# Kernel optimization log

Measured on AMD Instinct MI355X. Metric: run time of the kernel, lower is better.

## Reference

```python
import jax, jax.numpy as jnp
import numpy as np

B, OBS, T, H = 4096, 16, 32, 512  # batch, encoder length, decode seq_len, hidden_size


def _lstm_cell(x, h, c, Wi, Wh, b):
    # PyTorch gate order: i, f, g, o. b = b_ih + b_hh (mathematically identical).
    g = x @ Wi.T + h @ Wh.T + b
    i, f, gg, o = jnp.split(g, 4, axis=-1)
    c = jax.nn.sigmoid(f) * c + jax.nn.sigmoid(i) * jnp.tanh(gg)
    h = jax.nn.sigmoid(o) * jnp.tanh(c)
    return h, c


def _encode(xs, Wi, Wh, b):
    # xs: [B, T, 4]; returns final (h, c), zero initial state as in nn.LSTM.
    def step(carry, x):
        h, c = _lstm_cell(x, carry[0], carry[1], Wi, Wh, b)
        return (h, c), None
    z = jnp.zeros((xs.shape[0], H), xs.dtype)
    (h, c), _ = jax.lax.scan(step, (z, z), jnp.swapaxes(xs, 0, 1))
    return h, c


def setup_inputs() -> dict:
    key = jax.random.key(0)
    ks = jax.random.split(key, 22)
    s = 0.05
    p = lambda k, shape: (jax.random.normal(k, shape, jnp.float32) * s)
    return {
        "speed": jax.random.normal(ks[0], (B, OBS, 4), jnp.float32),
        "pos": jax.random.normal(ks[1], (B, OBS, 4), jnp.float32),
        "enc_s_Wi": p(ks[2], (4 * H, 4)), "enc_s_Wh": p(ks[3], (4 * H, H)), "enc_s_b": p(ks[4], (4 * H,)),
        "enc_p_Wi": p(ks[5], (4 * H, 4)), "enc_p_Wh": p(ks[6], (4 * H, H)), "enc_p_b": p(ks[7], (4 * H,)),
        "dec_s_Wi": p(ks[8], (4 * H, 4)), "dec_s_Wh": p(ks[9], (4 * H, H)), "dec_s_b": p(ks[10], (4 * H,)),
        "dec_i_Wi": p(ks[11], (4 * H, 4)), "dec_i_Wh": p(ks[12], (4 * H, H)), "dec_i_b": p(ks[13], (4 * H,)),
        "W_fs": p(ks[14], (4, H)), "b_fs": p(ks[15], (4,)),
        "W_fc": p(ks[16], (2, H)), "b_fc": p(ks[17], (2,)),
        "W_emb": p(ks[18], (4, 2)), "b_emb": p(ks[19], (4,)),
    }


def reference(speed, pos,
              enc_s_Wi, enc_s_Wh, enc_s_b,
              enc_p_Wi, enc_p_Wh, enc_p_b,
              dec_s_Wi, dec_s_Wh, dec_s_b,
              dec_i_Wi, dec_i_Wh, dec_i_b,
              W_fs, b_fs, W_fc, b_fc, W_emb, b_emb):
    h_se, c_se = _encode(speed, enc_s_Wi, enc_s_Wh, enc_s_b)
    h_pe, c_pe = _encode(pos, enc_p_Wi, enc_p_Wh, enc_p_b)
    h_s, c_s = h_se + h_pe, c_se + c_pe
    h_i, c_i = h_s, c_s
    last_speed = speed[:, -1, :]
    last_pos = pos[:, -1, :]

    def step(carry, _):
        h_s, c_s, h_i, c_i, ls, lp = carry
        h_s, c_s = _lstm_cell(ls, h_s, c_s, dec_s_Wi, dec_s_Wh, dec_s_b)
        h_i, c_i = _lstm_cell(lp, h_i, c_i, dec_i_Wi, dec_i_Wh, dec_i_b)
        sp = jnp.clip(h_s @ W_fs.T + b_fs, -100.0, 100.0)        # Hardtanh(-100, 100)
        it = jax.nn.relu(h_i @ W_fc.T + b_fc)                     # fc_crossing
        ls = jax.lax.stop_gradient(sp)                            # .detach()
        lp = jax.lax.stop_gradient(jax.nn.relu(it @ W_emb.T + b_emb))  # pos_embedding(.).detach()
        return (h_s, c_s, h_i, c_i, ls, lp), (sp, jax.nn.softmax(it, axis=1))

    carry0 = (h_s, c_s, h_i, c_i, last_speed, last_pos)
    _, (speed_seq, cross_seq) = jax.lax.scan(step, carry0, None, length=T)
    speed_outputs = jnp.swapaxes(speed_seq, 0, 1)   # [B, T, 4]
    # Faithful to the source bug: intention_outputs is never accumulated, so the
    # returned crossing_outputs holds ONLY the last step's softmax: [B, 1, 2].
    crossing_outputs = cross_seq[-1][:, None, :]
    return speed_outputs, crossing_outputs
```

## Files before the change

### kernel.cpp

```cpp
#include <hip/hip_runtime.h>
#include <stdint.h>

#define H 512
#define KAUG 528
#define KT_N 33
#define LROW 536
#define NROW 32
#define WMAT_ELEMS (16 * KT_N * 4 * 512)
#define WMAT8_BYTES 1081344
#define NTL8_BYTES 67584
#define T_DEC 32
#define B_TOT 4096
#define SCL 0.015625f

typedef __attribute__((ext_vector_type(8))) short short8;
typedef __attribute__((ext_vector_type(16))) float floatx16;
typedef __attribute__((ext_vector_type(2))) float float2v;
typedef __attribute__((ext_vector_type(4))) unsigned int uint4v;
typedef __attribute__((ext_vector_type(2))) unsigned int uint2v;

__device__ __forceinline__ unsigned short f2bf(float x) {
  union { float f; unsigned int u; } v; v.f = x;
  unsigned int u = v.u;
  return (unsigned short)((u + 0x7FFFu + ((u >> 16) & 1u)) >> 16);
}
__device__ __forceinline__ float bf2f(unsigned short s) {
  union { unsigned int u; float f; } v; v.u = ((unsigned int)s) << 16;
  return v.f;
}
__device__ __forceinline__ float rcpf(float x) { return __builtin_amdgcn_rcpf(x); }
__device__ __forceinline__ float sigm(float x) { return rcpf(1.0f + __expf(-x)); }
__device__ __forceinline__ float tanh_f(float x) {
  return 1.0f - 2.0f * rcpf(1.0f + __expf(2.0f * x));
}

__device__ __forceinline__ unsigned char f2e4m3(float f) {
  unsigned int u = __float_as_uint(f);
  unsigned int s = (u >> 24) & 0x80u;
  float a = fabsf(f);
  if (!(a < 464.0f)) return (unsigned char)(s | 0x7Eu);
  if (a < 0.0009765625f) return (unsigned char)s;
  int e = (int)((__float_as_uint(a) >> 23) & 0xFF) - 127;
  int q = (e < -6 ? -6 : e) - 3;
  float sc  = __uint_as_float((unsigned int)((127 - q) << 23));
  float isc = __uint_as_float((unsigned int)((127 + q) << 23));
  float n = rintf(a * sc);
  float r = n * isc;
  if (r == 0.0f) return (unsigned char)s;
  int e2 = (int)((__float_as_uint(r) >> 23) & 0xFF) - 127;
  unsigned int bits;
  if (e2 < -6) {
    bits = (unsigned int)(r * 512.0f + 0.5f);
  } else {
    float msc = __uint_as_float((unsigned int)((127 - (e2 - 3)) << 23));
    unsigned int mant = (unsigned int)(r * msc + 0.5f);
    bits = ((unsigned int)(e2 + 7) << 3) | (mant & 7u);
  }
  return (unsigned char)(s | bits);
}

__device__ __forceinline__ short8 dq8(unsigned int d0, unsigned int d1) {
  float2v p0 = __builtin_amdgcn_cvt_pk_f32_fp8(d0, false);
  float2v p1 = __builtin_amdgcn_cvt_pk_f32_fp8(d0, true);
  float2v p2 = __builtin_amdgcn_cvt_pk_f32_fp8(d1, false);
  float2v p3 = __builtin_amdgcn_cvt_pk_f32_fp8(d1, true);
  union { unsigned int u[4]; short8 s; } r;
  r.u[0] = __builtin_amdgcn_perm(__float_as_uint(p0[1]), __float_as_uint(p0[0]), 0x07060302u);
  r.u[1] = __builtin_amdgcn_perm(__float_as_uint(p1[1]), __float_as_uint(p1[0]), 0x07060302u);
  r.u[2] = __builtin_amdgcn_perm(__float_as_uint(p2[1]), __float_as_uint(p2[0]), 0x07060302u);
  r.u[3] = __builtin_amdgcn_perm(__float_as_uint(p3[1]), __float_as_uint(p3[0]), 0x07060302u);
  return r.s;
}

__global__ void prep_weights(
    const float* __restrict__ Wh_s, const float* __restrict__ Wi_s, const float* __restrict__ b_s,
    const float* __restrict__ Wh_p, const float* __restrict__ Wi_p, const float* __restrict__ b_p,
    short* __restrict__ wpack)
{
  int idx = blockIdx.x * 256 + threadIdx.x;
  const int per = 2048 * KAUG;
  if (idx >= 2 * per) return;
  int mat = idx / per;
  int rem = idx - mat * per;
  int n = rem / KAUG;
  int ka = rem - n * KAUG;
  const float* Wh = mat ? Wh_p : Wh_s;
  const float* Wi = mat ? Wi_p : Wi_s;
  const float* bb = mat ? b_p  : b_s;
  float v;
  if (ka < 512)      v = Wh[n * 512 + ka];
  else if (ka < 516) v = Wi[n * 4 + (ka - 512)];
  else if (ka == 516) v = bb[n];
  else               v = 0.0f;
  int g = n >> 9, ntL = (n >> 5) & 15, ni = n & 31;
  int kt = ka >> 4, kh = (ka >> 3) & 1, ks = ka & 7;
  int lanep = kh * 32 + ni;
  wpack[(size_t)mat * WMAT_ELEMS +
        (((((size_t)ntL * KT_N + kt) * 4 + g) << 9) + (lanep << 3) + ks)] = (short)f2bf(v);
}

__global__ void prep_fp8(
    const float* __restrict__ Wh_d, const float* __restrict__ Wi_d, const float* __restrict__ b_d,
    const float* __restrict__ Wh_i, const float* __restrict__ Wi_i, const float* __restrict__ b_i,
    unsigned char* __restrict__ wpack8)
{
  int idx = blockIdx.x * 256 + threadIdx.x;
  if (idx >= 2 * WMAT8_BYTES) return;
  int mat = idx / WMAT8_BYTES;
  int rem = idx - mat * WMAT8_BYTES;
  int ntL = rem / NTL8_BYTES;
  int off = rem - ntL * NTL8_BYTES;
  int g, lane, kt, ks;
  if (off < 65536) {
    int p = off >> 12;
    g = (off >> 10) & 3;
    lane = (off >> 4) & 63;
    int j = off & 15;
    kt = 2 * p + (j >> 3);
    ks = j & 7;
  } else {
    int t = off - 65536;
    g = t >> 9;
    lane = (t >> 3) & 63;
    ks = t & 7;
    kt = 32;
  }
  int n = g * 512 + ntL * 32 + (lane & 31);
  int ka = kt * 16 + (lane >> 5) * 8 + ks;
  const float* Wh = mat ? Wh_i : Wh_d;
  const float* Wi = mat ? Wi_i : Wi_d;
  const float* bb = mat ? b_i  : b_d;
  float v;
  if (ka < 512)       v = Wh[n * 512 + ka];
  else if (ka < 516)  v = Wi[n * 4 + (ka - 512)];
  else if (ka == 516) v = bb[n];
  else                v = 0.0f;
  wpack8[idx] = f2e4m3(v * 64.0f);
}

__device__ __forceinline__ void lstm_step_mfma(
    const short* hl, const short* __restrict__ wm,
    int lane, int wv, float c_reg[16], float hnew[16])
{
  int arow = lane & 31, ahalf = lane >> 5;
  const short* aptr = hl + arow * LROW + ahalf * 8;
  const short* bp = wm + (size_t)wv * (KT_N * 4 * 512) + (lane << 3);
  floatx16 ai = (floatx16)0.0f, af = (floatx16)0.0f, ag = (floatx16)0.0f, ao = (floatx16)0.0f;
  #pragma unroll 3
  for (int kt = 0; kt < KT_N; ++kt) {
    short8 a  = *(const short8*)(aptr + kt * 16);
    short8 b0 = *(const short8*)(bp);
    short8 b1 = *(const short8*)(bp + 512);
    short8 b2 = *(const short8*)(bp + 1024);
    short8 b3 = *(const short8*)(bp + 1536);
    bp += 2048;
    ai = __builtin_amdgcn_mfma_f32_32x32x16_bf16(a, b0, ai, 0, 0, 0);
    af = __builtin_amdgcn_mfma_f32_32x32x16_bf16(a, b1, af, 0, 0, 0);
    ag = __builtin_amdgcn_mfma_f32_32x32x16_bf16(a, b2, ag, 0, 0, 0);
    ao = __builtin_amdgcn_mfma_f32_32x32x16_bf16(a, b3, ao, 0, 0, 0);
  }
  #pragma unroll
  for (int r = 0; r < 16; ++r) {
    float si = sigm(ai[r]);
    float sf = sigm(af[r]);
    float tg = tanh_f(ag[r]);
    float so = sigm(ao[r]);
    float cn = sf * c_reg[r] + si * tg;
    c_reg[r] = cn;
    hnew[r] = so * tanh_f(cn);
  }
}

__device__ __forceinline__ void lstm_step_mfma_fp8(
    const short* hl, const unsigned char* __restrict__ wmb,
    int lane, int wv, float c_reg[16], float hnew[16])
{
  int arow = lane & 31, ahalf = lane >> 5;
  const short* aptr = hl + arow * LROW + ahalf * 8;
  const unsigned char* base = wmb + (size_t)wv * NTL8_BYTES;
  const uint4v* bp = (const uint4v*)(base + (lane << 4));
  floatx16 ai = (floatx16)0.0f, af = (floatx16)0.0f, ag = (floatx16)0.0f, ao = (floatx16)0.0f;
  #pragma unroll 1
  for (int p = 0; p < 16; ++p) {
    uint4v di = bp[0];
    uint4v df = bp[64];
    uint4v dg = bp[128];
    uint4v dd = bp[192];
    short8 a0 = *(const short8*)(aptr + p * 32);
    short8 a1 = *(const short8*)(aptr + p * 32 + 16);
    bp += 256;
    ai = __builtin_amdgcn_mfma_f32_32x32x16_bf16(a0, dq8(di[0], di[1]), ai, 0, 0, 0);
    af = __builtin_amdgcn_mfma_f32_32x32x16_bf16(a0, dq8(df[0], df[1]), af, 0, 0, 0);
    ag = __builtin_amdgcn_mfma_f32_32x32x16_bf16(a0, dq8(dg[0], dg[1]), ag, 0, 0, 0);
    ao = __builtin_amdgcn_mfma_f32_32x32x16_bf16(a0, dq8(dd[0], dd[1]), ao, 0, 0, 0);
    ai = __builtin_amdgcn_mfma_f32_32x32x16_bf16(a1, dq8(di[2], di[3]), ai, 0, 0, 0);
    af = __builtin_amdgcn_mfma_f32_32x32x16_bf16(a1, dq8(df[2], df[3]), af, 0, 0, 0);
    ag = __builtin_amdgcn_mfma_f32_32x32x16_bf16(a1, dq8(dg[2], dg[3]), ag, 0, 0, 0);
    ao = __builtin_amdgcn_mfma_f32_32x32x16_bf16(a1, dq8(dd[2], dd[3]), ao, 0, 0, 0);
  }
  {
    const uint2v* tp = (const uint2v*)(base + 65536 + (lane << 3));
    uint2v ti = tp[0], tf = tp[64], tg = tp[128], td = tp[192];
    short8 a0 = *(const short8*)(aptr + 512);
    ai = __builtin_amdgcn_mfma_f32_32x32x16_bf16(a0, dq8(ti[0], ti[1]), ai, 0, 0, 0);
    af = __builtin_amdgcn_mfma_f32_32x32x16_bf16(a0, dq8(tf[0], tf[1]), af, 0, 0, 0);
    ag = __builtin_amdgcn_mfma_f32_32x32x16_bf16(a0, dq8(tg[0], tg[1]), ag, 0, 0, 0);
    ao = __builtin_amdgcn_mfma_f32_32x32x16_bf16(a0, dq8(td[0], td[1]), ao, 0, 0, 0);
  }
  #pragma unroll
  for (int r = 0; r < 16; ++r) {
    float si = sigm(ai[r] * SCL);
    float sf = sigm(af[r] * SCL);
    float tg = tanh_f(ag[r] * SCL);
    float so = sigm(ao[r] * SCL);
    float cn = sf * c_reg[r] + si * tg;
    c_reg[r] = cn;
    hnew[r] = so * tanh_f(cn);
  }
}

__device__ __forceinline__ void write_h(short* hl, int lane, int wv, const float hnew[16]) {
  int arow = lane & 31, ahalf = lane >> 5;
  int col = (wv << 5) + arow;
  #pragma unroll
  for (int r = 0; r < 16; ++r) {
    int row = (r & 3) + ((r >> 2) << 3) + (ahalf << 2);
    hl[row * LROW + col] = (short)f2bf(hnew[r]);
  }
}

__global__ __launch_bounds__(1024) void lstm_encoder(
    const float* __restrict__ speed, const float* __restrict__ pos,
    const short* __restrict__ wpack,
    short* __restrict__ h_enc, float* __restrict__ c_enc)
{
  __shared__ short hl[NROW * LROW];
  int tid = threadIdx.x;
  int b = blockIdx.x;
  int xcd = b & 7, slot = b >> 3;
  int enc = xcd >> 2;
  int rg = slot * 4 + (xcd & 3);
  int r0 = rg * 32;
  const float* xin = enc ? pos : speed;
  const short* wm = wpack + (size_t)enc * WMAT_ELEMS;

  for (int i = tid; i < NROW * LROW; i += 1024) hl[i] = 0;
  __syncthreads();
  if (tid < 32) hl[tid * LROW + 516] = (short)0x3F80;
  if (tid < 128) {
    int r = tid >> 2, c = tid & 3;
    hl[r * LROW + 512 + c] = (short)f2bf(xin[(r0 + r) * 64 + c]);
  }
  __syncthreads();

  int lane = tid & 63, wv = tid >> 6;
  float c_reg[16];
  #pragma unroll
  for (int r = 0; r < 16; ++r) c_reg[r] = 0.0f;
  float hnew[16];

  for (int t = 0; t < 16; ++t) {
    lstm_step_mfma(hl, wm, lane, wv, c_reg, hnew);
    __syncthreads();
    write_h(hl, lane, wv, hnew);
    if (t < 15 && tid < 128) {
      int r = tid >> 2, c = tid & 3;
      hl[r * LROW + 512 + c] = (short)f2bf(xin[(r0 + r) * 64 + (t + 1) * 4 + c]);
    }
    __syncthreads();
  }

  for (int i = tid; i < 32 * 512; i += 1024) {
    int r = i >> 9, k = i & 511;
    h_enc[((size_t)(enc * B_TOT + r0 + r) << 9) + k] = hl[r * LROW + k];
  }
  int arow = lane & 31, ahalf = lane >> 5;
  int col = (wv << 5) + arow;
  #pragma unroll
  for (int r = 0; r < 16; ++r) {
    int row = (r & 3) + ((r >> 2) << 3) + (ahalf << 2);
    c_enc[((size_t)(enc * B_TOT + r0 + row) << 9) + col] = c_reg[r];
  }
}

__global__ __launch_bounds__(1024) void lstm_decoder(
    const float* __restrict__ speed, const float* __restrict__ pos,
    const unsigned char* __restrict__ wpack8,
    const short* __restrict__ h_enc, const float* __restrict__ c_enc,
    const float* __restrict__ W_fs, const float* __restrict__ b_fs,
    const float* __restrict__ W_fc, const float* __restrict__ b_fc,
    const float* __restrict__ W_emb, const float* __restrict__ b_emb,
    float* __restrict__ out)
{
  __shared__ short hl[NROW * LROW];
  int tid = threadIdx.x;
  int b = blockIdx.x;
  int xcd = b & 7, slot = b >> 3;
  int chain = xcd >> 2;
  int rg = slot * 4 + (xcd & 3);
  int r0 = rg * 32;
  const unsigned char* wm8 = wpack8 + (size_t)chain * WMAT8_BYTES;

  for (int i = tid; i < NROW * LROW; i += 1024) hl[i] = 0;
  __syncthreads();
  for (int i = tid; i < 32 * 512; i += 1024) {
    int r = i >> 9, k = i & 511;
    float h0 = bf2f((unsigned short)h_enc[((size_t)(r0 + r) << 9) + k])
             + bf2f((unsigned short)h_enc[((size_t)(B_TOT + r0 + r) << 9) + k]);
    hl[r * LROW + k] = (short)f2bf(h0);
  }
  if (tid < 32) hl[tid * LROW + 516] = (short)0x3F80;
  {
    const float* last = chain ? pos : speed;
    if (tid < 128) {
      int r = tid >> 2, c = tid & 3;
      hl[r * LROW + 512 + c] = (short)f2bf(last[(r0 + r) * 64 + 60 + c]);
    }
  }
  int lane = tid & 63, wv = tid >> 6;
  int arow = lane & 31, ahalf = lane >> 5;
  float c_reg[16];
  {
    int col = (wv << 5) + arow;
    #pragma unroll
    for (int r = 0; r < 16; ++r) {
      int row = (r & 3) + ((r >> 2) << 3) + (ahalf << 2);
      size_t gi = ((size_t)(r0 + row) << 9) + col;
      c_reg[r] = c_enc[gi] + c_enc[gi + (((size_t)B_TOT) << 9)];
    }
  }
  __syncthreads();

  float hnew[16];
  for (int t = 0; t < T_DEC; ++t) {
    lstm_step_mfma_fp8(hl, wm8, lane, wv, c_reg, hnew);
    __syncthreads();
    write_h(hl, lane, wv, hnew);
    __syncthreads();
    for (int r = 0; r < 2; ++r) {
      int row = wv * 2 + r;
      const short8 hvs = *(const short8*)(hl + row * LROW + lane * 8);
      float hv[8];
      #pragma unroll
      for (int j = 0; j < 8; ++j) hv[j] = bf2f((unsigned short)hvs[j]);
      if (chain == 0) {
        float p0 = 0.f, p1 = 0.f, p2 = 0.f, p3 = 0.f;
        #pragma unroll
        for (int j = 0; j < 8; ++j) {
          p0 += hv[j] * W_fs[0 * 512 + lane * 8 + j];
          p1 += hv[j] * W_fs[1 * 512 + lane * 8 + j];
          p2 += hv[j] * W_fs[2 * 512 + lane * 8 + j];
          p3 += hv[j] * W_fs[3 * 512 + lane * 8 + j];
        }
        #pragma unroll
        for (int off = 32; off > 0; off >>= 1) {
          p0 += __shfl_xor(p0, off);
          p1 += __shfl_xor(p1, off);
          p2 += __shfl_xor(p2, off);
          p3 += __shfl_xor(p3, off);
        }
        float s0 = fminf(fmaxf(p0 + b_fs[0], -100.0f), 100.0f);
        float s1 = fminf(fmaxf(p1 + b_fs[1], -100.0f), 100.0f);
        float s2 = fminf(fmaxf(p2 + b_fs[2], -100.0f), 100.0f);
        float s3 = fminf(fmaxf(p3 + b_fs[3], -100.0f), 100.0f);
        if (lane < 4) {
          float v = (lane == 0) ? s0 : (lane == 1) ? s1 : (lane == 2) ? s2 : s3;
          out[(size_t)(r0 + row) * 128 + t * 4 + lane] = v;
          hl[row * LROW + 512 + lane] = (short)f2bf(v);
        }
      } else {
        float p0 = 0.f, p1 = 0.f;
        #pragma unroll
        for (int j = 0; j < 8; ++j) {
          p0 += hv[j] * W_fc[0 * 512 + lane * 8 + j];
          p1 += hv[j] * W_fc[1 * 512 + lane * 8 + j];
        }
        #pragma unroll
        for (int off = 32; off > 0; off >>= 1) {
          p0 += __shfl_xor(p0, off);
          p1 += __shfl_xor(p1, off);
        }
        float it0 = fmaxf(p0 + b_fc[0], 0.0f);
        float it1 = fmaxf(p1 + b_fc[1], 0.0f);
        if (lane < 4) {
          float lp = fmaxf(W_emb[lane * 2] * it0 + W_emb[lane * 2 + 1] * it1 + b_emb[lane], 0.0f);
          hl[row * LROW + 512 + lane] = (short)f2bf(lp);
        }
        if (t == T_DEC - 1 && lane < 2) {
          float m = fmaxf(it0, it1);
          float e0 = __expf(it0 - m), e1 = __expf(it1 - m);
          float v = ((lane == 0) ? e0 : e1) * rcpf(e0 + e1);
          out[(size_t)524288 + (size_t)(r0 + row) * 2 + lane] = v;
        }
      }
    }
    __syncthreads();
  }
}

extern "C" void kernel_launch(void* const* d_in, const int* in_sizes, int n_in,
                              void* d_out, int out_size, void* d_ws, size_t ws_size,
                              hipStream_t stream)
{
  const float* speed    = (const float*)d_in[0];
  const float* pos      = (const float*)d_in[1];
  const float* enc_s_Wi = (const float*)d_in[2];
  const float* enc_s_Wh = (const float*)d_in[3];
  const float* enc_s_b  = (const float*)d_in[4];
  const float* enc_p_Wi = (const float*)d_in[5];
  const float* enc_p_Wh = (const float*)d_in[6];
  const float* enc_p_b  = (const float*)d_in[7];
  const float* dec_s_Wi = (const float*)d_in[8];
  const float* dec_s_Wh = (const float*)d_in[9];
  const float* dec_s_b  = (const float*)d_in[10];
  const float* dec_i_Wi = (const float*)d_in[11];
  const float* dec_i_Wh = (const float*)d_in[12];
  const float* dec_i_b  = (const float*)d_in[13];
  const float* W_fs     = (const float*)d_in[14];
  const float* b_fs     = (const float*)d_in[15];
  const float* W_fc     = (const float*)d_in[16];
  const float* b_fc     = (const float*)d_in[17];
  const float* W_emb    = (const float*)d_in[18];
  const float* b_emb    = (const float*)d_in[19];
  float* out = (float*)d_out;

  char* ws = (char*)d_ws;
  short* wpack          = (short*)ws;
  unsigned char* wpack8 = (unsigned char*)(ws + 4325376);
  short* h_enc          = (short*)(ws + 6488064);
  float* c_enc          = (float*)(ws + 14876672);

  prep_weights<<<8448, 256, 0, stream>>>(
      enc_s_Wh, enc_s_Wi, enc_s_b,
      enc_p_Wh, enc_p_Wi, enc_p_b,
      wpack);
  prep_fp8<<<8448, 256, 0, stream>>>(
      dec_s_Wh, dec_s_Wi, dec_s_b,
      dec_i_Wh, dec_i_Wi, dec_i_b,
      wpack8);
  lstm_encoder<<<256, 1024, 0, stream>>>(speed, pos, wpack, h_enc, c_enc);
  lstm_decoder<<<256, 1024, 0, stream>>>(speed, pos, wpack8, h_enc, c_enc,
                                         W_fs, b_fs, W_fc, b_fc, W_emb, b_emb, out);
}
```

Before: 1.377 ms.

## Split decoder into 16-row blocks with double-buffered hidden state

The decoder now launches 512 blocks of 512 threads instead of 256 of 1024. Each block handles 16 batch rows, and each wave computes two gate tiles. The hidden state is double-buffered in shared memory, so new h values are written straight into the next buffer and one barrier per step goes away. The trade-off is that the 32x32 MFMA tiles now carry only 16 valid rows (the rest are zero padding), and each block still streams the full FP8 weight matrix, so weight traffic and matrix work per useful row roughly double.

```diff
diff --git a/kernel.cpp b/kernel.cpp
--- a/kernel.cpp
+++ b/kernel.cpp
@@ -33,6 +33,8 @@
 __device__ __forceinline__ float tanh_f(float x) {
   return 1.0f - 2.0f * rcpf(1.0f + __expf(2.0f * x));
 }
+
+#define MFMA(A, B, C) __builtin_amdgcn_mfma_f32_32x32x16_bf16(A, B, C, 0, 0, 0)
 
 __device__ __forceinline__ unsigned char f2e4m3(float f) {
   unsigned int u = __float_as_uint(f);
@@ -72,7 +74,7 @@
   return r.s;
 }
 
-__global__ void prep_weights(
+__global__ void prep_enc(
     const float* __restrict__ Wh_s, const float* __restrict__ Wi_s, const float* __restrict__ b_s,
     const float* __restrict__ Wh_p, const float* __restrict__ Wi_p, const float* __restrict__ b_p,
     short* __restrict__ wpack)
@@ -154,10 +156,8 @@
     short8 b2 = *(const short8*)(bp + 1024);
     short8 b3 = *(const short8*)(bp + 1536);
     bp += 2048;
-    ai = __builtin_amdgcn_mfma_f32_32x32x16_bf16(a, b0, ai, 0, 0, 0);
-    af = __builtin_amdgcn_mfma_f32_32x32x16_bf16(a, b1, af, 0, 0, 0);
-    ag = __builtin_amdgcn_mfma_f32_32x32x16_bf16(a, b2, ag, 0, 0, 0);
-    ao = __builtin_amdgcn_mfma_f32_32x32x16_bf16(a, b3, ao, 0, 0, 0);
+    ai = MFMA(a, b0, ai); af = MFMA(a, b1, af);
+    ag = MFMA(a, b2, ag); ao = MFMA(a, b3, ao);
   }
   #pragma unroll
   for (int r = 0; r < 16; ++r) {
@@ -171,55 +171,7 @@
   }
 }
 
-__device__ __forceinline__ void lstm_step_mfma_fp8(
-    const short* hl, const unsigned char* __restrict__ wmb,
-    int lane, int wv, float c_reg[16], float hnew[16])
-{
-  int arow = lane & 31, ahalf = lane >> 5;
-  const short* aptr = hl + arow * LROW + ahalf * 8;
-  const unsigned char* base = wmb + (size_t)wv * NTL8_BYTES;
-  const uint4v* bp = (const uint4v*)(base + (lane << 4));
-  floatx16 ai = (floatx16)0.0f, af = (floatx16)0.0f, ag = (floatx16)0.0f, ao = (floatx16)0.0f;
-  #pragma unroll 1
-  for (int p = 0; p < 16; ++p) {
-    uint4v di = bp[0];
-    uint4v df = bp[64];
-    uint4v dg = bp[128];
-    uint4v dd = bp[192];
-    short8 a0 = *(const short8*)(aptr + p * 32);
-    short8 a1 = *(const short8*)(aptr + p * 32 + 16);
-    bp += 256;
-    ai = __builtin_amdgcn_mfma_f32_32x32x16_bf16(a0, dq8(di[0], di[1]), ai, 0, 0, 0);
-    af = __builtin_amdgcn_mfma_f32_32x32x16_bf16(a0, dq8(df[0], df[1]), af, 0, 0, 0);
-    ag = __builtin_amdgcn_mfma_f32_32x32x16_bf16(a0, dq8(dg[0], dg[1]), ag, 0, 0, 0);
-    ao = __builtin_amdgcn_mfma_f32_32x32x16_bf16(a0, dq8(dd[0], dd[1]), ao, 0, 0, 0);
-    ai = __builtin_amdgcn_mfma_f32_32x32x16_bf16(a1, dq8(di[2], di[3]), ai, 0, 0, 0);
-    af = __builtin_amdgcn_mfma_f32_32x32x16_bf16(a1, dq8(df[2], df[3]), af, 0, 0, 0);
-    ag = __builtin_amdgcn_mfma_f32_32x32x16_bf16(a1, dq8(dg[2], dg[3]), ag, 0, 0, 0);
-    ao = __builtin_amdgcn_mfma_f32_32x32x16_bf16(a1, dq8(dd[2], dd[3]), ao, 0, 0, 0);
-  }
-  {
-    const uint2v* tp = (const uint2v*)(base + 65536 + (lane << 3));
-    uint2v ti = tp[0], tf = tp[64], tg = tp[128], td = tp[192];
-    short8 a0 = *(const short8*)(aptr + 512);
-    ai = __builtin_amdgcn_mfma_f32_32x32x16_bf16(a0, dq8(ti[0], ti[1]), ai, 0, 0, 0);
-    af = __builtin_amdgcn_mfma_f32_32x32x16_bf16(a0, dq8(tf[0], tf[1]), af, 0, 0, 0);
-    ag = __builtin_amdgcn_mfma_f32_32x32x16_bf16(a0, dq8(tg[0], tg[1]), ag, 0, 0, 0);
-    ao = __builtin_amdgcn_mfma_f32_32x32x16_bf16(a0, dq8(td[0], td[1]), ao, 0, 0, 0);
-  }
-  #pragma unroll
-  for (int r = 0; r < 16; ++r) {
-    float si = sigm(ai[r] * SCL);
-    float sf = sigm(af[r] * SCL);
-    float tg = tanh_f(ag[r] * SCL);
-    float so = sigm(ao[r] * SCL);
-    float cn = sf * c_reg[r] + si * tg;
-    c_reg[r] = cn;
-    hnew[r] = so * tanh_f(cn);
-  }
-}
-
-__device__ __forceinline__ void write_h(short* hl, int lane, int wv, const float hnew[16]) {
+__device__ __forceinline__ void write_h16(short* hl, int lane, int wv, const float hnew[16]) {
   int arow = lane & 31, ahalf = lane >> 5;
   int col = (wv << 5) + arow;
   #pragma unroll
@@ -262,7 +214,7 @@
   for (int t = 0; t < 16; ++t) {
     lstm_step_mfma(hl, wm, lane, wv, c_reg, hnew);
     __syncthreads();
-    write_h(hl, lane, wv, hnew);
+    write_h16(hl, lane, wv, hnew);
     if (t < 15 && tid < 128) {
       int r = tid >> 2, c = tid & 3;
       hl[r * LROW + 512 + c] = (short)f2bf(xin[(r0 + r) * 64 + (t + 1) * 4 + c]);
@@ -283,7 +235,7 @@
   }
 }
 
-__global__ __launch_bounds__(1024) void lstm_decoder(
+__global__ __launch_bounds__(512, 4) void lstm_decoder(
     const float* __restrict__ speed, const float* __restrict__ pos,
     const unsigned char* __restrict__ wpack8,
     const short* __restrict__ h_enc, const float* __restrict__ c_enc,
@@ -292,54 +244,107 @@
     const float* __restrict__ W_emb, const float* __restrict__ b_emb,
     float* __restrict__ out)
 {
-  __shared__ short hl[NROW * LROW];
+  __shared__ short hl[2][NROW * LROW];
   int tid = threadIdx.x;
   int b = blockIdx.x;
-  int xcd = b & 7, slot = b >> 3;
-  int chain = xcd >> 2;
-  int rg = slot * 4 + (xcd & 3);
-  int r0 = rg * 32;
+  int chain = (b >> 8) & 1;
+  int r0 = (b & 255) * 16;
   const unsigned char* wm8 = wpack8 + (size_t)chain * WMAT8_BYTES;
-
-  for (int i = tid; i < NROW * LROW; i += 1024) hl[i] = 0;
+  int lane = tid & 63, wv = tid >> 6;
+  int arow = lane & 31, ahalf = lane >> 5;
+
+  {
+    short* hz = &hl[0][0];
+    for (int i = tid; i < 2 * NROW * LROW; i += 512) hz[i] = 0;
+  }
   __syncthreads();
-  for (int i = tid; i < 32 * 512; i += 1024) {
+  for (int i = tid; i < 16 * 512; i += 512) {
     int r = i >> 9, k = i & 511;
     float h0 = bf2f((unsigned short)h_enc[((size_t)(r0 + r) << 9) + k])
              + bf2f((unsigned short)h_enc[((size_t)(B_TOT + r0 + r) << 9) + k]);
-    hl[r * LROW + k] = (short)f2bf(h0);
-  }
-  if (tid < 32) hl[tid * LROW + 516] = (short)0x3F80;
+    hl[0][r * LROW + k] = (short)f2bf(h0);
+  }
+  if (tid < 32) hl[tid >> 4][(tid & 15) * LROW + 516] = (short)0x3F80;
   {
     const float* last = chain ? pos : speed;
-    if (tid < 128) {
+    if (tid < 64) {
       int r = tid >> 2, c = tid & 3;
-      hl[r * LROW + 512 + c] = (short)f2bf(last[(r0 + r) * 64 + 60 + c]);
+      hl[0][r * LROW + 512 + c] = (short)f2bf(last[(r0 + r) * 64 + 60 + c]);
     }
   }
-  int lane = tid & 63, wv = tid >> 6;
-  int arow = lane & 31, ahalf = lane >> 5;
-  float c_reg[16];
-  {
-    int col = (wv << 5) + arow;
+
+  float c_reg[2][8];
+  #pragma unroll
+  for (int jt = 0; jt < 2; ++jt) {
+    int col = (wv * 2 + jt) * 32 + arow;
     #pragma unroll
-    for (int r = 0; r < 16; ++r) {
+    for (int r = 0; r < 8; ++r) {
       int row = (r & 3) + ((r >> 2) << 3) + (ahalf << 2);
       size_t gi = ((size_t)(r0 + row) << 9) + col;
-      c_reg[r] = c_enc[gi] + c_enc[gi + (((size_t)B_TOT) << 9)];
+      c_reg[jt][r] = c_enc[gi] + c_enc[gi + ((size_t)B_TOT << 9)];
     }
   }
   __syncthreads();
 
-  float hnew[16];
   for (int t = 0; t < T_DEC; ++t) {
-    lstm_step_mfma_fp8(hl, wm8, lane, wv, c_reg, hnew);
+    const short* cb = hl[t & 1];
+    short* nb = &hl[(t + 1) & 1][0];
+    const short* aptr = cb + arow * LROW + ahalf * 8;
+
+    #pragma unroll
+    for (int jt = 0; jt < 2; ++jt) {
+      int ntL = wv * 2 + jt;
+      const unsigned char* base = wm8 + (size_t)ntL * NTL8_BYTES;
+      const uint4v* bp = (const uint4v*)(base + (lane << 4));
+      floatx16 ai = (floatx16)0.0f, af = (floatx16)0.0f,
+               ag = (floatx16)0.0f, ao = (floatx16)0.0f;
+      #pragma unroll 1
+      for (int p = 0; p < 16; ++p) {
+        uint4v di = bp[0];
+        uint4v df = bp[64];
+        uint4v dg = bp[128];
+        uint4v dd = bp[192];
+        short8 a0 = *(const short8*)(aptr + p * 32);
+        short8 a1 = *(const short8*)(aptr + p * 32 + 16);
+        bp += 256;
+        ai = MFMA(a0, dq8(di[0], di[1]), ai);
+        af = MFMA(a0, dq8(df[0], df[1]), af);
+        ag = MFMA(a0, dq8(dg[0], dg[1]), ag);
+        ao = MFMA(a0, dq8(dd[0], dd[1]), ao);
+        ai = MFMA(a1, dq8(di[2], di[3]), ai);
+        af = MFMA(a1, dq8(df[2], df[3]), af);
+        ag = MFMA(a1, dq8(dg[2], dg[3]), ag);
+        ao = MFMA(a1, dq8(dd[2], dd[3]), ao);
+      }
+      {
+        const uint2v* tp = (const uint2v*)(base + 65536 + (lane << 3));
+        uint2v ti = tp[0], tf = tp[64], tg2 = tp[128], td = tp[192];
+        short8 a0 = *(const short8*)(aptr + 512);
+        ai = MFMA(a0, dq8(ti[0], ti[1]), ai);
+        af = MFMA(a0, dq8(tf[0], tf[1]), af);
+        ag = MFMA(a0, dq8(tg2[0], tg2[1]), ag);
+        ao = MFMA(a0, dq8(td[0], td[1]), ao);
+      }
+      int col = ntL * 32 + arow;
+      #pragma unroll
+      for (int r = 0; r < 8; ++r) {
+        float si = sigm(ai[r] * SCL);
+        float sf = sigm(af[r] * SCL);
+        float tg = tanh_f(ag[r] * SCL);
+        float so = sigm(ao[r] * SCL);
+        float cn = sf * c_reg[jt][r] + si * tg;
+        c_reg[jt][r] = cn;
+        int row = (r & 3) + ((r >> 2) << 3) + (ahalf << 2);
+        nb[row * LROW + col] = (short)f2bf(so * tanh_f(cn));
+      }
+    }
     __syncthreads();
-    write_h(hl, lane, wv, hnew);
-    __syncthreads();
+
+    #pragma unroll 1
     for (int r = 0; r < 2; ++r) {
       int row = wv * 2 + r;
-      const short8 hvs = *(const short8*)(hl + row * LROW + lane * 8);
+      int grow = r0 + row;
+      const short8 hvs = *(const short8*)(nb + row * LROW + lane * 8);
       float hv[8];
       #pragma unroll
       for (int j = 0; j < 8; ++j) hv[j] = bf2f((unsigned short)hvs[j]);
@@ -365,8 +370,8 @@
         float s3 = fminf(fmaxf(p3 + b_fs[3], -100.0f), 100.0f);
         if (lane < 4) {
           float v = (lane == 0) ? s0 : (lane == 1) ? s1 : (lane == 2) ? s2 : s3;
-          out[(size_t)(r0 + row) * 128 + t * 4 + lane] = v;
-          hl[row * LROW + 512 + lane] = (short)f2bf(v);
+          out[(size_t)grow * 128 + t * 4 + lane] = v;
+          nb[row * LROW + 512 + lane] = (short)f2bf(v);
         }
       } else {
         float p0 = 0.f, p1 = 0.f;
@@ -384,13 +389,13 @@
         float it1 = fmaxf(p1 + b_fc[1], 0.0f);
         if (lane < 4) {
           float lp = fmaxf(W_emb[lane * 2] * it0 + W_emb[lane * 2 + 1] * it1 + b_emb[lane], 0.0f);
-          hl[row * LROW + 512 + lane] = (short)f2bf(lp);
+          nb[row * LROW + 512 + lane] = (short)f2bf(lp);
         }
         if (t == T_DEC - 1 && lane < 2) {
           float m = fmaxf(it0, it1);
           float e0 = __expf(it0 - m), e1 = __expf(it1 - m);
           float v = ((lane == 0) ? e0 : e1) * rcpf(e0 + e1);
-          out[(size_t)524288 + (size_t)(r0 + row) * 2 + lane] = v;
+          out[(size_t)524288 + (size_t)grow * 2 + lane] = v;
         }
       }
     }
@@ -430,7 +435,7 @@
   short* h_enc          = (short*)(ws + 6488064);
   float* c_enc          = (float*)(ws + 14876672);
 
-  prep_weights<<<8448, 256, 0, stream>>>(
+  prep_enc<<<8448, 256, 0, stream>>>(
       enc_s_Wh, enc_s_Wi, enc_s_b,
       enc_p_Wh, enc_p_Wi, enc_p_b,
       wpack);
@@ -439,6 +444,6 @@
       dec_i_Wh, dec_i_Wi, dec_i_b,
       wpack8);
   lstm_encoder<<<256, 1024, 0, stream>>>(speed, pos, wpack, h_enc, c_enc);
-  lstm_decoder<<<256, 1024, 0, stream>>>(speed, pos, wpack8, h_enc, c_enc,
-                                         W_fs, b_fs, W_fc, b_fc, W_emb, b_emb, out);
-}
+  lstm_decoder<<<512, 512, 0, stream>>>(speed, pos, wpack8, h_enc, c_enc,
+                                        W_fs, b_fs, W_fc, b_fc, W_emb, b_emb, out);
+}
```

After: 1.660 ms. +20.5%, slower.
